# Optimization experiments

Hardware: AMD Instinct MI355X
Metric: run time of the kernel (lower is better)

The kernel has to match this reference:

```python
import jax, jax.numpy as jnp
import numpy as np

B = 128          # batch of initial states
NUM_TRAJ = 128   # noise realizations per state
D = 16           # state dim (output_dim)
P = 5            # number of physical params
H = 64           # hidden width of the tiny drift/diffusion MLPs
DELTAT = 2.0 ** -8
MAXT = 0.25
STEPS = int(round(MAXT / DELTAT)) - 1   # 63 Euler-Maruyama steps (tvec has 64 points)
F = 1 + 2 * D + P                        # NN feature dim: [t, Re(x), Im(x), params]
N = B * NUM_TRAJ                         # total trajectories after tiling


def setup_inputs() -> dict:
    key = jax.random.key(0)
    ks = jax.random.split(key, 8)
    x_real = jax.random.normal(ks[0], (B, D), jnp.float32)
    x_imag = jax.random.normal(ks[1], (B, D), jnp.float32)
    params = jax.random.uniform(ks[2], (P,), jnp.float32)
    # Brownian increments dW ~ N(0, deltat), m=1 noise channel
    noise = jax.random.normal(ks[3], (N, STEPS, 1), jnp.float32) * float(np.sqrt(DELTAT))
    # Stacked weights for the 4 nets: [a_real, a_imag, b_real, b_imag]
    W1 = jax.random.normal(ks[4], (4, F, H), jnp.float32) / np.float32(np.sqrt(F))
    B1 = jax.random.normal(ks[5], (4, H), jnp.float32) * 0.01
    W2 = jax.random.normal(ks[6], (4, H, D), jnp.float32) / np.float32(np.sqrt(H)) * 0.5
    B2 = jax.random.normal(ks[7], (4, D), jnp.float32) * 0.01
    return {"x_real": x_real, "x_imag": x_imag, "params": params, "noise": noise,
            "W1": W1, "B1": B1, "W2": W2, "B2": B2}


def reference(x_real, x_imag, params, noise, W1, B1, W2, B2):
    # call(): tile params over batch, tile state over num_traj (input_param=-1 path)
    x = jax.lax.complex(x_real, x_imag)          # [B, D] complex64
    x = jnp.tile(x, (NUM_TRAJ, 1))               # [N, D]
    p = jnp.broadcast_to(params[None, :], (N, P))  # traj_inputs

    dt = jnp.float32(DELTAT)
    tvec = jnp.arange(STEPS, dtype=jnp.float32) * dt       # t_n for each Euler step
    dWs = jnp.swapaxes(noise, 0, 1)                          # [STEPS, N, 1]

    def nets(t, x):
        # NN drift/diffusion: features [t, Re(x), Im(x), params] -> 4 tiny MLPs at once
        feats = jnp.concatenate(
            [jnp.broadcast_to(t, (N, 1)), x.real, x.imag, p], axis=1)  # [N, F]
        h = jnp.tanh(jnp.einsum('nf,kfh->knh', feats, W1) + B1[:, None, :])
        o = jnp.einsum('knh,khd->knd', h, W2) + B2[:, None, :]          # [4, N, D]
        a = jax.lax.complex(o[0], o[1])   # drift,     [N, D]
        b = jax.lax.complex(o[2], o[3])   # diffusion, [N, D] (m=1)
        return a, b

    def step(x, inp):
        t, dw = inp                        # dw: [N, 1] real
        a, b = nets(t, x)
        x_next = x + a * dt + b * dw       # Euler-Maruyama
        return x_next, None

    xT, _ = jax.lax.scan(step, x, (tvec, dWs))
    # return final state y = xvec[:, -1] as concatenated real/imag parts [N, 2D]
    return jnp.concatenate([xT.real, xT.imag], axis=-1)
```

## Files before the change

kernel.cpp:

```cpp
#include <hip/hip_runtime.h>
#include <stdint.h>

#define NB    128
#define NSTEP 63
#define DT    0.00390625f
#define TSC   2.8853900817779268f

typedef __attribute__((ext_vector_type(8))) short bf16x8;
typedef __attribute__((ext_vector_type(4))) float f32x4;

union Frag { bf16x8 v; uint32_t u[4]; };

__device__ __forceinline__ short f2bf(float f) {
    uint32_t u = __float_as_uint(f);
    u += 0x7FFF + ((u >> 16) & 1);
    return (short)(u >> 16);
}

__device__ __forceinline__ uint32_t pk_bf16(float lo, float hi) {
    uint32_t r;
    asm("v_cvt_pk_bf16_f32 %0, %1, %2" : "=v"(r) : "v"(lo), "v"(hi));
    return r;
}

__device__ __forceinline__ float tanh_sc(float y) {
    float e = __builtin_amdgcn_exp2f(y);
    return fmaf(-2.0f, __builtin_amdgcn_rcpf(e + 1.0f), 1.0f);
}

__global__ __launch_bounds__(256, 4) void sde_mfma4(
    const float* __restrict__ x_real, const float* __restrict__ x_imag,
    const float* __restrict__ params, const float* __restrict__ noise,
    const float* __restrict__ W1, const float* __restrict__ B1,
    const float* __restrict__ W2, const float* __restrict__ B2,
    float* __restrict__ out)
{
    __shared__ __attribute__((aligned(16))) float xbuf[2][4][16][20];

    const int tid  = threadIdx.x;
    const int lane = tid & 63;
    const int l15  = lane & 15;
    const int g    = lane >> 4;
    const int wv   = tid >> 6;

    Frag w1f[4];
    #pragma unroll
    for (int t = 0; t < 4; ++t) {
        const int h = 16 * t + l15;
        #pragma unroll
        for (int j = 0; j < 8; ++j)
            w1f[t].v[j] = f2bf(TSC * W1[(wv * 38 + 1 + 8 * g + j) * 64 + h]);
    }

    Frag w2f[2];
    #pragma unroll
    for (int kt = 0; kt < 2; ++kt) {
        #pragma unroll
        for (int j = 0; j < 8; ++j) {
            const int hl = 16 * (2 * kt + (j >> 2)) + 4 * g + (j & 3);
            w2f[kt].v[j] = f2bf(W2[(wv * 64 + hl) * 16 + l15]);
        }
    }

    float pr[5];
    #pragma unroll
    for (int p = 0; p < 5; ++p) pr[p] = params[p];
    f32x4 biascur[4], wtdt[4];
    #pragma unroll
    for (int t = 0; t < 4; ++t) {
        #pragma unroll
        for (int r = 0; r < 4; ++r) {
            const int h = 16 * t + 4 * g + r;
            float b = B1[wv * 64 + h];
            #pragma unroll
            for (int p = 0; p < 5; ++p)
                b = fmaf(pr[p], W1[(wv * 38 + 33 + p) * 64 + h], b);
            biascur[t][r] = TSC * b;
            wtdt[t][r]    = (TSC * DT) * W1[(wv * 38 + 0) * 64 + h];
        }
    }

    f32x4 bc;
    #pragma unroll
    for (int r = 0; r < 4; ++r) bc[r] = B2[wv * 16 + 4 * g + r];

    const int n    = blockIdx.x * 16 + l15;
    const int xrow = n & (NB - 1);
    const float* __restrict__ xsrc = (g < 2) ? x_real : x_imag;
    float st[8];
    #pragma unroll
    for (int i = 0; i < 8; ++i) st[i] = xsrc[xrow * 16 + (g & 1) * 8 + i];

    const float* __restrict__ nsp = noise + (size_t)n * NSTEP;
    float dw = nsp[0];

    float* wrp           = &xbuf[0][wv][l15][4 * g];
    const float* rd_dr   = &xbuf[0][g >> 1][l15][8 * (g & 1)];
    const float* rd_df   = &xbuf[0][2 + (g >> 1)][l15][8 * (g & 1)];
    const int dstep = 4 * 16 * 20;

    for (int s = 0; s < NSTEP; ++s) {
        const float dwn = nsp[(s + 1 < NSTEP) ? s + 1 : s];

        Frag bx;
        bx.u[0] = pk_bf16(st[0], st[1]);
        bx.u[1] = pk_bf16(st[2], st[3]);
        bx.u[2] = pk_bf16(st[4], st[5]);
        bx.u[3] = pk_bf16(st[6], st[7]);

        f32x4 acc[4];
        #pragma unroll
        for (int t = 0; t < 4; ++t)
            acc[t] = __builtin_amdgcn_mfma_f32_16x16x32_bf16(
                w1f[t].v, bx.v, biascur[t], 0, 0, 0);
        #pragma unroll
        for (int t = 0; t < 4; ++t) biascur[t] += wtdt[t];

        f32x4 o = bc;
        #pragma unroll
        for (int kt = 0; kt < 2; ++kt) {
            const float t0 = tanh_sc(acc[2 * kt][0]);
            const float t1 = tanh_sc(acc[2 * kt][1]);
            const float t2 = tanh_sc(acc[2 * kt][2]);
            const float t3 = tanh_sc(acc[2 * kt][3]);
            const float t4 = tanh_sc(acc[2 * kt + 1][0]);
            const float t5 = tanh_sc(acc[2 * kt + 1][1]);
            const float t6 = tanh_sc(acc[2 * kt + 1][2]);
            const float t7 = tanh_sc(acc[2 * kt + 1][3]);
            Frag pb;
            pb.u[0] = pk_bf16(t0, t1);  pb.u[1] = pk_bf16(t2, t3);
            pb.u[2] = pk_bf16(t4, t5);  pb.u[3] = pk_bf16(t6, t7);
            o = __builtin_amdgcn_mfma_f32_16x16x32_bf16(w2f[kt].v, pb.v, o, 0, 0, 0);
        }

        const int db = s & 1;
        *reinterpret_cast<f32x4*>(wrp + db * dstep) = o;
        __syncthreads();
        const float* dp = rd_dr + db * dstep;
        const float* fp = rd_df + db * dstep;
        const f32x4 dr0 = *reinterpret_cast<const f32x4*>(dp);
        const f32x4 dr1 = *reinterpret_cast<const f32x4*>(dp + 4);
        const f32x4 df0 = *reinterpret_cast<const f32x4*>(fp);
        const f32x4 df1 = *reinterpret_cast<const f32x4*>(fp + 4);

        #pragma unroll
        for (int i = 0; i < 4; ++i) {
            st[i]     = fmaf(DT, dr0[i], fmaf(dw, df0[i], st[i]));
            st[i + 4] = fmaf(DT, dr1[i], fmaf(dw, df1[i], st[i + 4]));
        }
        dw = dwn;
    }

    if (wv == 0) {
        float4* op = reinterpret_cast<float4*>(out + (size_t)n * 32 + 8 * g);
        op[0] = make_float4(st[0], st[1], st[2], st[3]);
        op[1] = make_float4(st[4], st[5], st[6], st[7]);
    }
}

extern "C" void kernel_launch(void* const* d_in, const int* in_sizes, int n_in,
                              void* d_out, int out_size, void* d_ws, size_t ws_size,
                              hipStream_t stream) {
    const float* x_real = (const float*)d_in[0];
    const float* x_imag = (const float*)d_in[1];
    const float* params = (const float*)d_in[2];
    const float* noise  = (const float*)d_in[3];
    const float* W1     = (const float*)d_in[4];
    const float* B1     = (const float*)d_in[5];
    const float* W2     = (const float*)d_in[6];
    const float* B2     = (const float*)d_in[7];
    float* out = (float*)d_out;

    sde_mfma4<<<dim3(1024), dim3(256), 0, stream>>>(
        x_real, x_imag, params, noise, W1, B1, W2, B2, out);
}
```

Before: 83.43 us.

## Process two trajectory tiles per block to interleave independent MFMA chains

Each block now handles 32 trajectories as two independent 16-row tiles, A and B, and halves the grid to 512 blocks. Interleaving the two independent MFMA/tanh dependency chains per step is meant to hide MFMA and transcendental latency and to amortize each __syncthreads over twice the work. The tanh is rewritten in a paired float2 form, and the state update uses vector FMAs. In exchange, register use and LDS size double, the occupancy hint is removed, and the grid has fewer blocks, which may reduce occupancy.

After: 89.91 us. 1.08x slower.

```diff
diff --git a/kernel.cpp b/kernel.cpp
--- a/kernel.cpp
+++ b/kernel.cpp
@@ -8,6 +8,7 @@
 
 typedef __attribute__((ext_vector_type(8))) short bf16x8;
 typedef __attribute__((ext_vector_type(4))) float f32x4;
+typedef __attribute__((ext_vector_type(2))) float f32x2;
 
 union Frag { bf16x8 v; uint32_t u[4]; };
 
@@ -23,19 +24,21 @@
     return r;
 }
 
-__device__ __forceinline__ float tanh_sc(float y) {
-    float e = __builtin_amdgcn_exp2f(y);
-    return fmaf(-2.0f, __builtin_amdgcn_rcpf(e + 1.0f), 1.0f);
-}
-
-__global__ __launch_bounds__(256, 4) void sde_mfma4(
+__device__ __forceinline__ f32x2 tanh2_sc(float y0, float y1) {
+    f32x2 e = { __builtin_amdgcn_exp2f(y0), __builtin_amdgcn_exp2f(y1) };
+    f32x2 ep = e + (f32x2)1.0f;
+    f32x2 r = { __builtin_amdgcn_rcpf(ep.x), __builtin_amdgcn_rcpf(ep.y) };
+    return __builtin_elementwise_fma(r, (f32x2)(-2.0f), (f32x2)(1.0f));
+}
+
+__global__ __launch_bounds__(256) void sde_mfma8(
     const float* __restrict__ x_real, const float* __restrict__ x_imag,
     const float* __restrict__ params, const float* __restrict__ noise,
     const float* __restrict__ W1, const float* __restrict__ B1,
     const float* __restrict__ W2, const float* __restrict__ B2,
     float* __restrict__ out)
 {
-    __shared__ __attribute__((aligned(16))) float xbuf[2][4][16][20];
+    __shared__ __attribute__((aligned(16))) float xbuf[2][2][4][16][20];
 
     const int tid  = threadIdx.x;
     const int lane = tid & 63;
@@ -84,77 +87,109 @@
     #pragma unroll
     for (int r = 0; r < 4; ++r) bc[r] = B2[wv * 16 + 4 * g + r];
 
-    const int n    = blockIdx.x * 16 + l15;
-    const int xrow = n & (NB - 1);
+    const int nA = blockIdx.x * 32 + l15;
+    const int nB = nA + 16;
     const float* __restrict__ xsrc = (g < 2) ? x_real : x_imag;
-    float st[8];
-    #pragma unroll
-    for (int i = 0; i < 8; ++i) st[i] = xsrc[xrow * 16 + (g & 1) * 8 + i];
-
-    const float* __restrict__ nsp = noise + (size_t)n * NSTEP;
-    float dw = nsp[0];
-
-    float* wrp           = &xbuf[0][wv][l15][4 * g];
-    const float* rd_dr   = &xbuf[0][g >> 1][l15][8 * (g & 1)];
-    const float* rd_df   = &xbuf[0][2 + (g >> 1)][l15][8 * (g & 1)];
-    const int dstep = 4 * 16 * 20;
+    const int xoff = (g & 1) * 8;
+    f32x4 stAlo = *reinterpret_cast<const f32x4*>(&xsrc[(nA & (NB - 1)) * 16 + xoff]);
+    f32x4 stAhi = *reinterpret_cast<const f32x4*>(&xsrc[(nA & (NB - 1)) * 16 + xoff + 4]);
+    f32x4 stBlo = *reinterpret_cast<const f32x4*>(&xsrc[(nB & (NB - 1)) * 16 + xoff]);
+    f32x4 stBhi = *reinterpret_cast<const f32x4*>(&xsrc[(nB & (NB - 1)) * 16 + xoff + 4]);
+
+    const float* __restrict__ nspA = noise + (size_t)nA * NSTEP;
+    const float* __restrict__ nspB = noise + (size_t)nB * NSTEP;
+    float dwA = nspA[0], dwB = nspB[0];
+
+    const int dstep = 2 * 4 * 16 * 20;
+    const int gstep = 4 * 16 * 20;
+    float* wrpA         = &xbuf[0][0][wv][l15][4 * g];
+    const float* rd_drA = &xbuf[0][0][g >> 1][l15][8 * (g & 1)];
+    const float* rd_dfA = &xbuf[0][0][2 + (g >> 1)][l15][8 * (g & 1)];
 
     for (int s = 0; s < NSTEP; ++s) {
-        const float dwn = nsp[(s + 1 < NSTEP) ? s + 1 : s];
-
-        Frag bx;
-        bx.u[0] = pk_bf16(st[0], st[1]);
-        bx.u[1] = pk_bf16(st[2], st[3]);
-        bx.u[2] = pk_bf16(st[4], st[5]);
-        bx.u[3] = pk_bf16(st[6], st[7]);
-
-        f32x4 acc[4];
+        const int sn = (s + 1 < NSTEP) ? s + 1 : s;
+        const float dwAn = nspA[sn], dwBn = nspB[sn];
+
+        Frag bxA;
+        bxA.u[0] = pk_bf16(stAlo[0], stAlo[1]);
+        bxA.u[1] = pk_bf16(stAlo[2], stAlo[3]);
+        bxA.u[2] = pk_bf16(stAhi[0], stAhi[1]);
+        bxA.u[3] = pk_bf16(stAhi[2], stAhi[3]);
+        Frag bxB;
+        bxB.u[0] = pk_bf16(stBlo[0], stBlo[1]);
+        bxB.u[1] = pk_bf16(stBlo[2], stBlo[3]);
+        bxB.u[2] = pk_bf16(stBhi[0], stBhi[1]);
+        bxB.u[3] = pk_bf16(stBhi[2], stBhi[3]);
+
+        f32x4 accA[4], accB[4];
         #pragma unroll
         for (int t = 0; t < 4; ++t)
-            acc[t] = __builtin_amdgcn_mfma_f32_16x16x32_bf16(
-                w1f[t].v, bx.v, biascur[t], 0, 0, 0);
+            accA[t] = __builtin_amdgcn_mfma_f32_16x16x32_bf16(
+                w1f[t].v, bxA.v, biascur[t], 0, 0, 0);
+        #pragma unroll
+        for (int t = 0; t < 4; ++t)
+            accB[t] = __builtin_amdgcn_mfma_f32_16x16x32_bf16(
+                w1f[t].v, bxB.v, biascur[t], 0, 0, 0);
         #pragma unroll
         for (int t = 0; t < 4; ++t) biascur[t] += wtdt[t];
 
-        f32x4 o = bc;
+        f32x4 oA = bc, oB = bc;
         #pragma unroll
         for (int kt = 0; kt < 2; ++kt) {
-            const float t0 = tanh_sc(acc[2 * kt][0]);
-            const float t1 = tanh_sc(acc[2 * kt][1]);
-            const float t2 = tanh_sc(acc[2 * kt][2]);
-            const float t3 = tanh_sc(acc[2 * kt][3]);
-            const float t4 = tanh_sc(acc[2 * kt + 1][0]);
-            const float t5 = tanh_sc(acc[2 * kt + 1][1]);
-            const float t6 = tanh_sc(acc[2 * kt + 1][2]);
-            const float t7 = tanh_sc(acc[2 * kt + 1][3]);
-            Frag pb;
-            pb.u[0] = pk_bf16(t0, t1);  pb.u[1] = pk_bf16(t2, t3);
-            pb.u[2] = pk_bf16(t4, t5);  pb.u[3] = pk_bf16(t6, t7);
-            o = __builtin_amdgcn_mfma_f32_16x16x32_bf16(w2f[kt].v, pb.v, o, 0, 0, 0);
+            const f32x2 a0 = tanh2_sc(accA[2 * kt][0],     accA[2 * kt][1]);
+            const f32x2 a1 = tanh2_sc(accA[2 * kt][2],     accA[2 * kt][3]);
+            const f32x2 a2 = tanh2_sc(accA[2 * kt + 1][0], accA[2 * kt + 1][1]);
+            const f32x2 a3 = tanh2_sc(accA[2 * kt + 1][2], accA[2 * kt + 1][3]);
+            Frag pbA;
+            pbA.u[0] = pk_bf16(a0.x, a0.y);  pbA.u[1] = pk_bf16(a1.x, a1.y);
+            pbA.u[2] = pk_bf16(a2.x, a2.y);  pbA.u[3] = pk_bf16(a3.x, a3.y);
+            oA = __builtin_amdgcn_mfma_f32_16x16x32_bf16(w2f[kt].v, pbA.v, oA, 0, 0, 0);
+
+            const f32x2 b0 = tanh2_sc(accB[2 * kt][0],     accB[2 * kt][1]);
+            const f32x2 b1 = tanh2_sc(accB[2 * kt][2],     accB[2 * kt][3]);
+            const f32x2 b2 = tanh2_sc(accB[2 * kt + 1][0], accB[2 * kt + 1][1]);
+            const f32x2 b3 = tanh2_sc(accB[2 * kt + 1][2], accB[2 * kt + 1][3]);
+            Frag pbB;
+            pbB.u[0] = pk_bf16(b0.x, b0.y);  pbB.u[1] = pk_bf16(b1.x, b1.y);
+            pbB.u[2] = pk_bf16(b2.x, b2.y);  pbB.u[3] = pk_bf16(b3.x, b3.y);
+            oB = __builtin_amdgcn_mfma_f32_16x16x32_bf16(w2f[kt].v, pbB.v, oB, 0, 0, 0);
         }
 
         const int db = s & 1;
-        *reinterpret_cast<f32x4*>(wrp + db * dstep) = o;
+        *reinterpret_cast<f32x4*>(wrpA + db * dstep)         = oA;
+        *reinterpret_cast<f32x4*>(wrpA + db * dstep + gstep) = oB;
         __syncthreads();
-        const float* dp = rd_dr + db * dstep;
-        const float* fp = rd_df + db * dstep;
-        const f32x4 dr0 = *reinterpret_cast<const f32x4*>(dp);
-        const f32x4 dr1 = *reinterpret_cast<const f32x4*>(dp + 4);
-        const f32x4 df0 = *reinterpret_cast<const f32x4*>(fp);
-        const f32x4 df1 = *reinterpret_cast<const f32x4*>(fp + 4);
-
-        #pragma unroll
-        for (int i = 0; i < 4; ++i) {
-            st[i]     = fmaf(DT, dr0[i], fmaf(dw, df0[i], st[i]));
-            st[i + 4] = fmaf(DT, dr1[i], fmaf(dw, df1[i], st[i + 4]));
-        }
-        dw = dwn;
+        const float* dpA = rd_drA + db * dstep;
+        const float* fpA = rd_dfA + db * dstep;
+        const f32x4 drA0 = *reinterpret_cast<const f32x4*>(dpA);
+        const f32x4 drA1 = *reinterpret_cast<const f32x4*>(dpA + 4);
+        const f32x4 dfA0 = *reinterpret_cast<const f32x4*>(fpA);
+        const f32x4 dfA1 = *reinterpret_cast<const f32x4*>(fpA + 4);
+        const f32x4 drB0 = *reinterpret_cast<const f32x4*>(dpA + gstep);
+        const f32x4 drB1 = *reinterpret_cast<const f32x4*>(dpA + gstep + 4);
+        const f32x4 dfB0 = *reinterpret_cast<const f32x4*>(fpA + gstep);
+        const f32x4 dfB1 = *reinterpret_cast<const f32x4*>(fpA + gstep + 4);
+
+        const f32x4 dt4 = (f32x4)DT;
+        const f32x4 dwA4 = (f32x4)dwA, dwB4 = (f32x4)dwB;
+        stAlo = __builtin_elementwise_fma(dt4, drA0,
+                __builtin_elementwise_fma(dwA4, dfA0, stAlo));
+        stAhi = __builtin_elementwise_fma(dt4, drA1,
+                __builtin_elementwise_fma(dwA4, dfA1, stAhi));
+        stBlo = __builtin_elementwise_fma(dt4, drB0,
+                __builtin_elementwise_fma(dwB4, dfB0, stBlo));
+        stBhi = __builtin_elementwise_fma(dt4, drB1,
+                __builtin_elementwise_fma(dwB4, dfB1, stBhi));
+        dwA = dwAn; dwB = dwBn;
     }
 
     if (wv == 0) {
-        float4* op = reinterpret_cast<float4*>(out + (size_t)n * 32 + 8 * g);
-        op[0] = make_float4(st[0], st[1], st[2], st[3]);
-        op[1] = make_float4(st[4], st[5], st[6], st[7]);
+        float4* opA = reinterpret_cast<float4*>(out + (size_t)nA * 32 + 8 * g);
+        opA[0] = make_float4(stAlo[0], stAlo[1], stAlo[2], stAlo[3]);
+        opA[1] = make_float4(stAhi[0], stAhi[1], stAhi[2], stAhi[3]);
+        float4* opB = reinterpret_cast<float4*>(out + (size_t)nB * 32 + 8 * g);
+        opB[0] = make_float4(stBlo[0], stBlo[1], stBlo[2], stBlo[3]);
+        opB[1] = make_float4(stBhi[0], stBhi[1], stBhi[2], stBhi[3]);
     }
 }
 
@@ -171,6 +206,6 @@
     const float* B2     = (const float*)d_in[7];
     float* out = (float*)d_out;
 
-    sde_mfma4<<<dim3(1024), dim3(256), 0, stream>>>(
+    sde_mfma8<<<dim3(512), dim3(256), 0, stream>>>(
         x_real, x_imag, params, noise, W1, B1, W2, B2, out);
 }
```

## Compute all four MLPs within one wave per trajectory tile, removing LDS exchange

Applied to the files above, without the earlier changes.

Before, four waves each computed one of the four nets for the same 16 trajectories and swapped drift/diffusion through LDS with a __syncthreads every step. Now each wave computes all four nets (16 first-layer and 8 second-layer MFMAs) for its own 16 trajectories, so the Euler update uses registers only with no shared memory or barrier. The grid drops from 1024 to 256 blocks and the tanh is written as paired vector ops. Each thread now holds far more weight fragments, biases and accumulators, which raises register pressure and lowers occupancy and latency hiding.

Result: no change. 85.07 us (+2.0%).

```diff
diff --git a/kernel.cpp b/kernel.cpp
--- a/kernel.cpp
+++ b/kernel.cpp
@@ -8,6 +8,7 @@
 
 typedef __attribute__((ext_vector_type(8))) short bf16x8;
 typedef __attribute__((ext_vector_type(4))) float f32x4;
+typedef __attribute__((ext_vector_type(2))) float f32x2;
 
 union Frag { bf16x8 v; uint32_t u[4]; };
 
@@ -23,139 +24,136 @@
     return r;
 }
 
-__device__ __forceinline__ float tanh_sc(float y) {
-    float e = __builtin_amdgcn_exp2f(y);
-    return fmaf(-2.0f, __builtin_amdgcn_rcpf(e + 1.0f), 1.0f);
+__device__ __forceinline__ f32x2 tanh2_sc(float y0, float y1) {
+    f32x2 e = { __builtin_amdgcn_exp2f(y0), __builtin_amdgcn_exp2f(y1) };
+    f32x2 ep = e + (f32x2)1.0f;
+    f32x2 r = { __builtin_amdgcn_rcpf(ep.x), __builtin_amdgcn_rcpf(ep.y) };
+    return __builtin_elementwise_fma(r, (f32x2)(-2.0f), (f32x2)(1.0f));
 }
 
-__global__ __launch_bounds__(256, 4) void sde_mfma4(
+__global__ __launch_bounds__(256, 1) void sde_1wave(
     const float* __restrict__ x_real, const float* __restrict__ x_imag,
     const float* __restrict__ params, const float* __restrict__ noise,
     const float* __restrict__ W1, const float* __restrict__ B1,
     const float* __restrict__ W2, const float* __restrict__ B2,
     float* __restrict__ out)
 {
-    __shared__ __attribute__((aligned(16))) float xbuf[2][4][16][20];
-
     const int tid  = threadIdx.x;
     const int lane = tid & 63;
     const int l15  = lane & 15;
     const int g    = lane >> 4;
     const int wv   = tid >> 6;
+    const int wid  = blockIdx.x * 4 + wv;
+    const int n    = wid * 16 + l15;
 
-    Frag w1f[4];
+    Frag w1f[16];
     #pragma unroll
-    for (int t = 0; t < 4; ++t) {
-        const int h = 16 * t + l15;
+    for (int t = 0; t < 16; ++t) {
+        const int net = t >> 2;
+        const int hn  = 16 * (t & 3) + l15;
         #pragma unroll
-        for (int j = 0; j < 8; ++j)
-            w1f[t].v[j] = f2bf(TSC * W1[(wv * 38 + 1 + 8 * g + j) * 64 + h]);
+        for (int j = 0; j < 8; ++j) {
+            const int jf = (j < 4) ? (4 * g + j) : (16 + 4 * g + (j - 4));
+            w1f[t].v[j] = f2bf(TSC * W1[(net * 38 + 1 + jf) * 64 + hn]);
+        }
     }
 
-    Frag w2f[2];
+    Frag w2f[4][2];
     #pragma unroll
-    for (int kt = 0; kt < 2; ++kt) {
+    for (int k = 0; k < 4; ++k)
         #pragma unroll
-        for (int j = 0; j < 8; ++j) {
-            const int hl = 16 * (2 * kt + (j >> 2)) + 4 * g + (j & 3);
-            w2f[kt].v[j] = f2bf(W2[(wv * 64 + hl) * 16 + l15]);
-        }
-    }
+        for (int kt = 0; kt < 2; ++kt)
+            #pragma unroll
+            for (int j = 0; j < 8; ++j) {
+                const int hl = 16 * (2 * kt + (j >> 2)) + 4 * g + (j & 3);
+                w2f[k][kt].v[j] = f2bf(W2[(k * 64 + hl) * 16 + l15]);
+            }
 
     float pr[5];
     #pragma unroll
     for (int p = 0; p < 5; ++p) pr[p] = params[p];
-    f32x4 biascur[4], wtdt[4];
+    f32x4 biascur[16], wtdt[16];
     #pragma unroll
-    for (int t = 0; t < 4; ++t) {
+    for (int t = 0; t < 16; ++t) {
         #pragma unroll
         for (int r = 0; r < 4; ++r) {
-            const int h = 16 * t + 4 * g + r;
-            float b = B1[wv * 64 + h];
+            const int c1 = 16 * t + 4 * g + r;
+            const int net = c1 >> 6, h = c1 & 63;
+            float b = B1[net * 64 + h];
             #pragma unroll
             for (int p = 0; p < 5; ++p)
-                b = fmaf(pr[p], W1[(wv * 38 + 33 + p) * 64 + h], b);
+                b = fmaf(pr[p], W1[(net * 38 + 33 + p) * 64 + h], b);
             biascur[t][r] = TSC * b;
-            wtdt[t][r]    = (TSC * DT) * W1[(wv * 38 + 0) * 64 + h];
+            wtdt[t][r]    = (TSC * DT) * W1[(net * 38 + 0) * 64 + h];
         }
     }
 
-    f32x4 bc;
+    f32x4 bc[4];
     #pragma unroll
-    for (int r = 0; r < 4; ++r) bc[r] = B2[wv * 16 + 4 * g + r];
+    for (int k = 0; k < 4; ++k)
+        #pragma unroll
+        for (int r = 0; r < 4; ++r) bc[k][r] = B2[k * 16 + 4 * g + r];
 
-    const int n    = blockIdx.x * 16 + l15;
     const int xrow = n & (NB - 1);
-    const float* __restrict__ xsrc = (g < 2) ? x_real : x_imag;
-    float st[8];
-    #pragma unroll
-    for (int i = 0; i < 8; ++i) st[i] = xsrc[xrow * 16 + (g & 1) * 8 + i];
+    f32x4 sre = *reinterpret_cast<const f32x4*>(&x_real[xrow * 16 + 4 * g]);
+    f32x4 sim = *reinterpret_cast<const f32x4*>(&x_imag[xrow * 16 + 4 * g]);
 
     const float* __restrict__ nsp = noise + (size_t)n * NSTEP;
     float dw = nsp[0];
-
-    float* wrp           = &xbuf[0][wv][l15][4 * g];
-    const float* rd_dr   = &xbuf[0][g >> 1][l15][8 * (g & 1)];
-    const float* rd_df   = &xbuf[0][2 + (g >> 1)][l15][8 * (g & 1)];
-    const int dstep = 4 * 16 * 20;
 
     for (int s = 0; s < NSTEP; ++s) {
         const float dwn = nsp[(s + 1 < NSTEP) ? s + 1 : s];
 
         Frag bx;
-        bx.u[0] = pk_bf16(st[0], st[1]);
-        bx.u[1] = pk_bf16(st[2], st[3]);
-        bx.u[2] = pk_bf16(st[4], st[5]);
-        bx.u[3] = pk_bf16(st[6], st[7]);
+        bx.u[0] = pk_bf16(sre[0], sre[1]);
+        bx.u[1] = pk_bf16(sre[2], sre[3]);
+        bx.u[2] = pk_bf16(sim[0], sim[1]);
+        bx.u[3] = pk_bf16(sim[2], sim[3]);
 
-        f32x4 acc[4];
+        f32x4 acc[16];
         #pragma unroll
-        for (int t = 0; t < 4; ++t)
+        for (int t = 0; t < 16; ++t)
             acc[t] = __builtin_amdgcn_mfma_f32_16x16x32_bf16(
                 w1f[t].v, bx.v, biascur[t], 0, 0, 0);
         #pragma unroll
-        for (int t = 0; t < 4; ++t) biascur[t] += wtdt[t];
+        for (int t = 0; t < 16; ++t) biascur[t] += wtdt[t];
 
-        f32x4 o = bc;
+        f32x4 th[16];
         #pragma unroll
-        for (int kt = 0; kt < 2; ++kt) {
-            const float t0 = tanh_sc(acc[2 * kt][0]);
-            const float t1 = tanh_sc(acc[2 * kt][1]);
-            const float t2 = tanh_sc(acc[2 * kt][2]);
-            const float t3 = tanh_sc(acc[2 * kt][3]);
-            const float t4 = tanh_sc(acc[2 * kt + 1][0]);
-            const float t5 = tanh_sc(acc[2 * kt + 1][1]);
-            const float t6 = tanh_sc(acc[2 * kt + 1][2]);
-            const float t7 = tanh_sc(acc[2 * kt + 1][3]);
-            Frag pb;
-            pb.u[0] = pk_bf16(t0, t1);  pb.u[1] = pk_bf16(t2, t3);
-            pb.u[2] = pk_bf16(t4, t5);  pb.u[3] = pk_bf16(t6, t7);
-            o = __builtin_amdgcn_mfma_f32_16x16x32_bf16(w2f[kt].v, pb.v, o, 0, 0, 0);
+        for (int t = 0; t < 16; ++t) {
+            const f32x2 lo = tanh2_sc(acc[t][0], acc[t][1]);
+            const f32x2 hi = tanh2_sc(acc[t][2], acc[t][3]);
+            th[t][0] = lo.x; th[t][1] = lo.y; th[t][2] = hi.x; th[t][3] = hi.y;
         }
 
-        const int db = s & 1;
-        *reinterpret_cast<f32x4*>(wrp + db * dstep) = o;
-        __syncthreads();
-        const float* dp = rd_dr + db * dstep;
-        const float* fp = rd_df + db * dstep;
-        const f32x4 dr0 = *reinterpret_cast<const f32x4*>(dp);
-        const f32x4 dr1 = *reinterpret_cast<const f32x4*>(dp + 4);
-        const f32x4 df0 = *reinterpret_cast<const f32x4*>(fp);
-        const f32x4 df1 = *reinterpret_cast<const f32x4*>(fp + 4);
+        f32x4 o[4];
+        #pragma unroll
+        for (int k = 0; k < 4; ++k) {
+            o[k] = bc[k];
+            #pragma unroll
+            for (int kt = 0; kt < 2; ++kt) {
+                const int T0 = 4 * k + 2 * kt;
+                Frag pb;
+                pb.u[0] = pk_bf16(th[T0][0],     th[T0][1]);
+                pb.u[1] = pk_bf16(th[T0][2],     th[T0][3]);
+                pb.u[2] = pk_bf16(th[T0 + 1][0], th[T0 + 1][1]);
+                pb.u[3] = pk_bf16(th[T0 + 1][2], th[T0 + 1][3]);
+                o[k] = __builtin_amdgcn_mfma_f32_16x16x32_bf16(
+                    w2f[k][kt].v, pb.v, o[k], 0, 0, 0);
+            }
+        }
 
-        #pragma unroll
-        for (int i = 0; i < 4; ++i) {
-            st[i]     = fmaf(DT, dr0[i], fmaf(dw, df0[i], st[i]));
-            st[i + 4] = fmaf(DT, dr1[i], fmaf(dw, df1[i], st[i + 4]));
-        }
+        const f32x4 dt4 = (f32x4)DT;
+        const f32x4 dw4 = (f32x4)dw;
+        sre = __builtin_elementwise_fma(dt4, o[0],
+              __builtin_elementwise_fma(dw4, o[2], sre));
+        sim = __builtin_elementwise_fma(dt4, o[1],
+              __builtin_elementwise_fma(dw4, o[3], sim));
         dw = dwn;
     }
 
-    if (wv == 0) {
-        float4* op = reinterpret_cast<float4*>(out + (size_t)n * 32 + 8 * g);
-        op[0] = make_float4(st[0], st[1], st[2], st[3]);
-        op[1] = make_float4(st[4], st[5], st[6], st[7]);
-    }
+    *reinterpret_cast<f32x4*>(out + (size_t)n * 32 + 4 * g)      = sre;
+    *reinterpret_cast<f32x4*>(out + (size_t)n * 32 + 16 + 4 * g) = sim;
 }
 
 extern "C" void kernel_launch(void* const* d_in, const int* in_sizes, int n_in,
@@ -171,6 +169,6 @@
     const float* B2     = (const float*)d_in[7];
     float* out = (float*)d_out;
 
-    sde_mfma4<<<dim3(1024), dim3(256), 0, stream>>>(
+    sde_1wave<<<dim3(256), dim3(256), 0, stream>>>(
         x_real, x_imag, params, noise, W1, B1, W2, B2, out);
 }
```
